# Kernel optimization log

Hardware: AMD Instinct MI355X
Metric: run time of the kernel (lower is better)

Reference implementation:

```python
import jax, jax.numpy as jnp
import numpy as np

B, H, K, D = 4096, 3, 32768, 128


def setup_inputs() -> dict:
    key = jax.random.key(0)
    k_in, k_emb = jax.random.split(key)
    inputs = jax.random.normal(k_in, (B, 1, D), dtype=jnp.float32)
    # xavier-uniform-ish init with per-head decay 0.5**h (gain 6.0), as in the module
    ks = jax.random.split(k_emb, H)
    tables = []
    for h in range(H):
        gain = 6.0 * (0.5 ** h)
        bound = gain * np.sqrt(6.0 / (K + D))
        tables.append(jax.random.uniform(ks[h], (K, D), jnp.float32, -bound, bound))
    emb = jnp.stack(tables, axis=0)  # [H, K, D]
    return {"inputs": inputs, "emb": emb}


def reference(inputs, emb):
    # Eval-mode HRQ forward: per-head negative squared-L2 distances to the
    # codebook on the running residual, hard argmax assignment, summed codes.
    x = inputs[:, 0, :]                      # [B, D]
    n_heads = emb.shape[0]
    resid = x
    quantized = jnp.zeros_like(x)
    codes = []
    for h in range(n_heads):
        W = emb[h]                            # [K, D]
        # -(||r||^2 + ||w||^2 - 2 r.w)  -> argmax == nearest code
        dists = -(jnp.sum(resid * resid, axis=1, keepdims=True)
                  + jnp.sum(W * W, axis=1)
                  - 2.0 * resid @ W.T)        # [B, K]
        c = jnp.argmax(dists, axis=-1)        # [B]
        q = jnp.take(W, c, axis=0)            # onehot(c) @ W == gather
        resid = resid - q
        quantized = quantized + q
        codes.append(c)
    loss = jnp.zeros(x.shape[0], dtype=inputs.dtype)
    return loss, quantized.reshape(inputs.shape), jnp.stack(codes, axis=1)
```

## Files before the change

### kernel.cpp

```cpp
#include <hip/hip_runtime.h>
#include <math.h>

#define NB 4096
#define NH 3
#define NK 32768
#define ND 128
#define KE 384
#define KA 256
#define RB 64
#define CS 16
#define CPB (NK / CS)
#define CI 256
#define NCI (CPB / CI)

typedef _Float16 half8_t __attribute__((ext_vector_type(8)));
typedef _Float16 half2_t __attribute__((ext_vector_type(2)));
typedef float f32x4 __attribute__((ext_vector_type(4)));
typedef __attribute__((address_space(1))) const unsigned int gu32_t;
typedef __attribute__((address_space(3))) unsigned int lu32_t;

__global__ __launch_bounds__(64) void init_kernel(const float* __restrict__ inp,
                                                  float* __restrict__ resid,
                                                  float* __restrict__ rr,
                                                  float* __restrict__ out,
                                                  _Float16* __restrict__ Aext) {
  int row = blockIdx.x;
  int lane = threadIdx.x;
  const float2* ip = (const float2*)(inp + row * ND);
  float2 v = ip[lane];
  ((float2*)(resid + row * ND))[lane] = v;
  ((float2*)(out + NB + row * ND))[lane] = make_float2(0.f, 0.f);
  if (lane == 0) out[row] = 0.f;
  _Float16 h0 = (_Float16)v.x, h1 = (_Float16)v.y;
  _Float16 l0 = (_Float16)(v.x - (float)h0), l1 = (_Float16)(v.y - (float)h1);
  half2_t h = {h0, h1}, l = {l0, l1};
  _Float16* base = Aext + (size_t)row * KA;
  *(half2_t*)(base + 2 * lane) = h;
  *(half2_t*)(base + 128 + 2 * lane) = l;
  float s = v.x * v.x + v.y * v.y;
  #pragma unroll
  for (int m = 32; m; m >>= 1) s += __shfl_xor(s, m, 64);
  if (lane == 0) rr[row] = s;
}

__global__ __launch_bounds__(256) void norms_kernel(const float* __restrict__ emb,
                                                    float* __restrict__ norms) {
  int row = blockIdx.x * 4 + (threadIdx.x >> 6);
  int lane = threadIdx.x & 63;
  const float2* wp = (const float2*)(emb + (size_t)row * ND);
  float2 v = wp[lane];
  float s = v.x * v.x + v.y * v.y;
  #pragma unroll
  for (int m = 32; m; m >>= 1) s += __shfl_xor(s, m, 64);
  if (lane == 0) norms[row] = s;
}

__global__ __launch_bounds__(256) void split_w_kernel(const float* __restrict__ W,
                                                      _Float16* __restrict__ Bext) {
  const int cg = blockIdx.x;
  const int n_lo = threadIdx.x & 15;
  const int c = threadIdx.x >> 4;
  const int n = cg * 16 + n_lo;

  const float4* wp = (const float4*)(W + (size_t)n * ND + c * 8);
  float4 v0 = wp[0], v1 = wp[1];
  float xv[8] = {v0.x, v0.y, v0.z, v0.w, v1.x, v1.y, v1.z, v1.w};
  half8_t h, l;
  #pragma unroll
  for (int j = 0; j < 8; ++j) {
    _Float16 hh = (_Float16)xv[j];
    h[j] = hh;
    l[j] = (_Float16)(xv[j] - (float)hh);
  }
  const int ks0 = c >> 2;
  const int klo = c & 3;
  _Float16* base = Bext + (size_t)(cg >> 2) * 24576 + (cg & 3) * 512 + klo * 128 + n_lo * 8;
  *(half8_t*)(base + ks0 * 2048) = h;
  *(half8_t*)(base + (4 + ks0) * 2048) = l;
  *(half8_t*)(base + (8 + ks0) * 2048) = h;
}

__global__ __launch_bounds__(256, 2) void score_mfma_kernel(
    const _Float16* __restrict__ Aext, const _Float16* __restrict__ Bext,
    const float* __restrict__ rr, const float* __restrict__ normh,
    float* __restrict__ partial_s, int* __restrict__ partial_i) {
  __shared__ __align__(16) _Float16 Ash[RB * KA];

  const int bid = blockIdx.x;
  const int cs = bid & 15;
  const int rowb = bid >> 4;
  const int rowBase = rowb * RB;
  const int colBase0 = cs * CPB;

  const int tid = threadIdx.x;
  const int lane = tid & 63;
  const int wn = tid >> 6;
  const int l15 = lane & 15;
  const int q = lane >> 4;

  {
    const int mrow = lane >> 3;
    const int cg = (lane & 7) ^ (mrow & 7);
    #pragma unroll
    for (int i = 0; i < 8; ++i) {
      int wc = wn * 8 + i;
      int p = wc >> 3;
      int m0 = (wc & 7) * 8;
      const _Float16* gA = Aext + (size_t)(rowBase + m0 + mrow) * KA + p * 64 + cg * 8;
      __builtin_amdgcn_global_load_lds((gu32_t*)gA, (lu32_t*)&Ash[(p * 64 + m0) * 64], 16, 0, 0);
    }
  }

  int aaddr[2][4];
  #pragma unroll
  for (int par = 0; par < 2; ++par)
    #pragma unroll
    for (int mt = 0; mt < 4; ++mt) {
      int m = mt * 16 + l15;
      int slot = (par * 4 + q) ^ (m & 7);
      aaddr[par][mt] = (m * 8 + slot) * 16;
    }

  float rv[16];
  #pragma unroll
  for (int mt = 0; mt < 4; ++mt)
    #pragma unroll
    for (int reg = 0; reg < 4; ++reg)
      rv[mt * 4 + reg] = rr[rowBase + mt * 16 + q * 4 + reg];

  float bs[16];
  int bi[16];
  #pragma unroll
  for (int t = 0; t < 16; ++t) { bs[t] = -INFINITY; bi[t] = 0x7fffffff; }

  __syncthreads();

  #pragma unroll 1
  for (int ci = NCI - 1; ci >= 0; --ci) {
    const int ncol = colBase0 + ci * CI + wn * 64;
    const unsigned int boff = (unsigned int)(ncol >> 6) * 24576u + (unsigned int)lane * 8u;

    f32x4 acc[4][4];
    #pragma unroll
    for (int i = 0; i < 4; ++i)
      #pragma unroll
      for (int j = 0; j < 4; ++j) acc[i][j] = (f32x4){0.f, 0.f, 0.f, 0.f};

    #pragma unroll 4
    for (int ks = 0; ks < 12; ++ks) {
      half8_t bf[4];
      #pragma unroll
      for (int tn = 0; tn < 4; ++tn)
        bf[tn] = *(const half8_t*)(Bext + boff + (unsigned int)(ks * 2048 + tn * 512));
      const int ka = (ks & 3) | ((ks >> 1) & 4);
      half8_t af[4];
      #pragma unroll
      for (int mt = 0; mt < 4; ++mt)
        af[mt] = *(const half8_t*)((const char*)Ash + aaddr[ka & 1][mt] + (ka >> 1) * 8192);
      #pragma unroll
      for (int mt = 0; mt < 4; ++mt)
        #pragma unroll
        for (int tn = 0; tn < 4; ++tn)
          acc[mt][tn] = __builtin_amdgcn_mfma_f32_16x16x32_f16(af[mt], bf[tn], acc[mt][tn], 0, 0, 0);
    }

    #pragma unroll
    for (int tn = 3; tn >= 0; --tn) {
      float nw = normh[ncol + tn * 16 + l15];
      int cidx = ncol + tn * 16 + l15;
      #pragma unroll
      for (int mt = 0; mt < 4; ++mt) {
        #pragma unroll
        for (int reg = 0; reg < 4; ++reg) {
          const int s = mt * 4 + reg;
          float t1 = rv[s] + nw;
          float v = fmaf(2.0f, acc[mt][tn][reg], -t1);
          if (v >= bs[s]) { bs[s] = v; bi[s] = cidx; }
        }
      }
    }
  }

  __syncthreads();
  float* red_s = (float*)Ash;
  int* red_i = (int*)Ash + RB * 4;
  #pragma unroll
  for (int t = 0; t < 16; ++t) {
    float s = bs[t];
    int ii = bi[t];
    #pragma unroll
    for (int mask = 1; mask <= 8; mask <<= 1) {
      float os = __shfl_xor(s, mask, 64);
      int oi = __shfl_xor(ii, mask, 64);
      if (os > s || (os == s && oi < ii)) { s = os; ii = oi; }
    }
    if (l15 == 0) {
      int rloc = (t >> 2) * 16 + q * 4 + (t & 3);
      red_s[rloc * 4 + wn] = s;
      red_i[rloc * 4 + wn] = ii;
    }
  }
  __syncthreads();
  if (tid < RB) {
    float s0 = red_s[tid * 4];
    int i0 = red_i[tid * 4];
    #pragma unroll
    for (int x = 1; x < 4; ++x) {
      float sx = red_s[tid * 4 + x];
      int ix = red_i[tid * 4 + x];
      if (sx > s0 || (sx == s0 && ix < i0)) { s0 = sx; i0 = ix; }
    }
    partial_s[(size_t)(rowBase + tid) * CS + cs] = s0;
    partial_i[(size_t)(rowBase + tid) * CS + cs] = i0;
  }
}

__global__ __launch_bounds__(64) void reduce_update_kernel(const float* __restrict__ embh,
                                                           float* __restrict__ resid,
                                                           float* __restrict__ rr,
                                                           const float* __restrict__ ps,
                                                           const int* __restrict__ pi,
                                                           float* __restrict__ out,
                                                           _Float16* __restrict__ Aext, int h) {
  int row = blockIdx.x;
  int lane = threadIdx.x;
  float bs = -INFINITY;
  int bi = 0x7fffffff;
  if (lane < CS) {
    bs = ps[(size_t)row * CS + lane];
    bi = pi[(size_t)row * CS + lane];
  }
  #pragma unroll
  for (int m = 8; m; m >>= 1) {
    float os = __shfl_xor(bs, m, 64);
    int oi = __shfl_xor(bi, m, 64);
    if (os > bs || (os == bs && oi < bi)) { bs = os; bi = oi; }
  }
  int c = __shfl(bi, 0, 64);
  if (lane == 0) out[NB + NB * ND + row * NH + h] = (float)c;

  const float* wv = embh + (size_t)c * ND;
  float q0 = wv[lane], q1 = wv[lane + 64];
  float r0 = resid[row * ND + lane] - q0;
  float r1 = resid[row * ND + lane + 64] - q1;
  resid[row * ND + lane] = r0;
  resid[row * ND + lane + 64] = r1;
  out[NB + row * ND + lane] += q0;
  out[NB + row * ND + lane + 64] += q1;

  _Float16 h0 = (_Float16)r0, l0 = (_Float16)(r0 - (float)h0);
  _Float16 h1 = (_Float16)r1, l1 = (_Float16)(r1 - (float)h1);
  _Float16* ab = Aext + (size_t)row * KA;
  ab[lane] = h0;       ab[lane + 64] = h1;
  ab[128 + lane] = l0; ab[128 + lane + 64] = l1;

  float s = r0 * r0 + r1 * r1;
  #pragma unroll
  for (int m = 32; m; m >>= 1) s += __shfl_xor(s, m, 64);
  if (lane == 0) rr[row] = s;
}

extern "C" void kernel_launch(void* const* d_in, const int* in_sizes, int n_in,
                              void* d_out, int out_size, void* d_ws, size_t ws_size,
                              hipStream_t stream) {
  const float* inp = (const float*)d_in[0];
  const float* emb = (const float*)d_in[1];
  float* out = (float*)d_out;

  float* resid = (float*)d_ws;
  float* rr = resid + NB * ND;
  float* norms = rr + NB;
  float* ps = norms + NH * NK;
  int* pi = (int*)(ps + (size_t)NB * CS);
  _Float16* Aext = (_Float16*)(pi + (size_t)NB * CS);
  _Float16* Bext = Aext + (size_t)NB * KA;

  hipLaunchKernelGGL(init_kernel, dim3(NB), dim3(64), 0, stream, inp, resid, rr, out, Aext);
  hipLaunchKernelGGL(norms_kernel, dim3(NH * NK / 4), dim3(256), 0, stream, emb, norms);
  for (int h = 0; h < NH; ++h) {
    hipLaunchKernelGGL(split_w_kernel, dim3(NK / 16), dim3(256), 0, stream,
                       emb + (size_t)h * NK * ND, Bext);
    hipLaunchKernelGGL(score_mfma_kernel, dim3((NB / RB) * CS), dim3(256), 0, stream,
                       Aext, Bext, rr, norms + (size_t)h * NK, ps, pi);
    hipLaunchKernelGGL(reduce_update_kernel, dim3(NB), dim3(64), 0, stream,
                       emb + (size_t)h * NK * ND, resid, rr, ps, pi, out, Aext, h);
  }
}
```

Measured before the change: 470.4 us.

## Drop duplicated hi B slab and convert all heads' codebooks in one launch

```diff
diff --git a/kernel.cpp b/kernel.cpp
--- a/kernel.cpp
+++ b/kernel.cpp
@@ -5,8 +5,8 @@
 #define NH 3
 #define NK 32768
 #define ND 128
-#define KE 384
 #define KA 256
+#define KB 256
 #define RB 64
 #define CS 16
 #define CPB (NK / CS)
@@ -55,14 +55,15 @@
   if (lane == 0) norms[row] = s;
 }
 
-__global__ __launch_bounds__(256) void split_w_kernel(const float* __restrict__ W,
-                                                      _Float16* __restrict__ Bext) {
-  const int cg = blockIdx.x;
+__global__ __launch_bounds__(256) void split_w_all_kernel(const float* __restrict__ emb,
+                                                          _Float16* __restrict__ Bext) {
+  const int head = blockIdx.x >> 11;
+  const int cg = blockIdx.x & 2047;
   const int n_lo = threadIdx.x & 15;
   const int c = threadIdx.x >> 4;
   const int n = cg * 16 + n_lo;
 
-  const float4* wp = (const float4*)(W + (size_t)n * ND + c * 8);
+  const float4* wp = (const float4*)(emb + (size_t)head * NK * ND + (size_t)n * ND + c * 8);
   float4 v0 = wp[0], v1 = wp[1];
   float xv[8] = {v0.x, v0.y, v0.z, v0.w, v1.x, v1.y, v1.z, v1.w};
   half8_t h, l;
@@ -74,10 +75,10 @@
   }
   const int ks0 = c >> 2;
   const int klo = c & 3;
-  _Float16* base = Bext + (size_t)(cg >> 2) * 24576 + (cg & 3) * 512 + klo * 128 + n_lo * 8;
+  _Float16* base = Bext + (size_t)head * NK * KB + (size_t)(cg >> 2) * 16384 +
+                   (cg & 3) * 512 + klo * 128 + n_lo * 8;
   *(half8_t*)(base + ks0 * 2048) = h;
   *(half8_t*)(base + (4 + ks0) * 2048) = l;
-  *(half8_t*)(base + (8 + ks0) * 2048) = h;
 }
 
 __global__ __launch_bounds__(256, 2) void score_mfma_kernel(
@@ -138,7 +139,7 @@
   #pragma unroll 1
   for (int ci = NCI - 1; ci >= 0; --ci) {
     const int ncol = colBase0 + ci * CI + wn * 64;
-    const unsigned int boff = (unsigned int)(ncol >> 6) * 24576u + (unsigned int)lane * 8u;
+    const unsigned int boff = (unsigned int)(ncol >> 6) * 16384u + (unsigned int)lane * 8u;
 
     f32x4 acc[4][4];
     #pragma unroll
@@ -146,22 +147,36 @@
       #pragma unroll
       for (int j = 0; j < 4; ++j) acc[i][j] = (f32x4){0.f, 0.f, 0.f, 0.f};
 
-    #pragma unroll 4
-    for (int ks = 0; ks < 12; ++ks) {
-      half8_t bf[4];
-      #pragma unroll
-      for (int tn = 0; tn < 4; ++tn)
-        bf[tn] = *(const half8_t*)(Bext + boff + (unsigned int)(ks * 2048 + tn * 512));
-      const int ka = (ks & 3) | ((ks >> 1) & 4);
-      half8_t af[4];
-      #pragma unroll
-      for (int mt = 0; mt < 4; ++mt)
-        af[mt] = *(const half8_t*)((const char*)Ash + aaddr[ka & 1][mt] + (ka >> 1) * 8192);
+    #pragma unroll 2
+    for (int kc = 0; kc < 4; ++kc) {
+      half8_t bh[4], bl[4];
+      #pragma unroll
+      for (int tn = 0; tn < 4; ++tn) {
+        bh[tn] = *(const half8_t*)(Bext + boff + (unsigned int)(kc * 2048 + tn * 512));
+        bl[tn] = *(const half8_t*)(Bext + boff + (unsigned int)((4 + kc) * 2048 + tn * 512));
+      }
+      const int par = kc & 1, p = kc >> 1;
+      half8_t afh[4], afl[4];
+      #pragma unroll
+      for (int mt = 0; mt < 4; ++mt) {
+        afh[mt] = *(const half8_t*)((const char*)Ash + aaddr[par][mt] + p * 8192);
+        afl[mt] = *(const half8_t*)((const char*)Ash + aaddr[par][mt] + 16384 + p * 8192);
+      }
       #pragma unroll
       for (int mt = 0; mt < 4; ++mt)
         #pragma unroll
         for (int tn = 0; tn < 4; ++tn)
-          acc[mt][tn] = __builtin_amdgcn_mfma_f32_16x16x32_f16(af[mt], bf[tn], acc[mt][tn], 0, 0, 0);
+          acc[mt][tn] = __builtin_amdgcn_mfma_f32_16x16x32_f16(afh[mt], bh[tn], acc[mt][tn], 0, 0, 0);
+      #pragma unroll
+      for (int mt = 0; mt < 4; ++mt)
+        #pragma unroll
+        for (int tn = 0; tn < 4; ++tn)
+          acc[mt][tn] = __builtin_amdgcn_mfma_f32_16x16x32_f16(afl[mt], bh[tn], acc[mt][tn], 0, 0, 0);
+      #pragma unroll
+      for (int mt = 0; mt < 4; ++mt)
+        #pragma unroll
+        for (int tn = 0; tn < 4; ++tn)
+          acc[mt][tn] = __builtin_amdgcn_mfma_f32_16x16x32_f16(afh[mt], bl[tn], acc[mt][tn], 0, 0, 0);
     }
 
     #pragma unroll
@@ -277,11 +292,10 @@
 
   hipLaunchKernelGGL(init_kernel, dim3(NB), dim3(64), 0, stream, inp, resid, rr, out, Aext);
   hipLaunchKernelGGL(norms_kernel, dim3(NH * NK / 4), dim3(256), 0, stream, emb, norms);
+  hipLaunchKernelGGL(split_w_all_kernel, dim3(NH * NK / 16), dim3(256), 0, stream, emb, Bext);
   for (int h = 0; h < NH; ++h) {
-    hipLaunchKernelGGL(split_w_kernel, dim3(NK / 16), dim3(256), 0, stream,
-                       emb + (size_t)h * NK * ND, Bext);
     hipLaunchKernelGGL(score_mfma_kernel, dim3((NB / RB) * CS), dim3(256), 0, stream,
-                       Aext, Bext, rr, norms + (size_t)h * NK, ps, pi);
+                       Aext, Bext + (size_t)h * NK * KB, rr, norms + (size_t)h * NK, ps, pi);
     hipLaunchKernelGGL(reduce_update_kernel, dim3(NB), dim3(64), 0, stream,
                        emb + (size_t)h * NK * ND, resid, rr, ps, pi, out, Aext, h);
   }
```

New measurement: 405.6 us. 1.16x faster.
